# Kernel tuning notes

Measured on AMD Instinct MI355X. Metric: run time of the kernel, lower is better.

The kernel has to match this reference:

```python
import jax, jax.numpy as jnp
import numpy as np

BSZ, SEQ, D, NHEAD, NLAYER, DFF, NQ = 4, 48, 256, 2, 2, 2048, 512
LN_EPS = 1e-5
NEG = jnp.float32(-1e30)


def _layernorm(x, w, b):
    m = jnp.mean(x, axis=-1, keepdims=True)
    v = jnp.mean((x - m) ** 2, axis=-1, keepdims=True)
    return (x - m) / jnp.sqrt(v + LN_EPS) * w + b


def _span_max(x):
    # Cumulative span max: span[b,s,e] = max(x[b,s:e+1]) for e>=s, else 0.
    B, S, H = x.shape
    padded = jnp.concatenate([x, jnp.full((B, S, H), NEG, x.dtype)], axis=1)  # [B,2S,H]

    def step(tmp, i):
        shifted = jax.lax.dynamic_slice(padded, (0, i, 0), (B, S, H))  # x shifted left by i, padded with -inf
        tmp = jnp.maximum(tmp, shifted)  # tmp[b,s] = max(x[b,s:s+i+1])
        return tmp, tmp

    _, ys = jax.lax.scan(step, jnp.full((B, S, H), NEG, x.dtype), jnp.arange(S))
    # ys: [width, B, start, H]; span[b,s,e] = ys[e-s, b, s]
    si = jnp.arange(S)[:, None]
    ei = jnp.arange(S)[None, :]
    w = jnp.clip(ei - si, 0, S - 1)
    span = ys[w, :, jnp.broadcast_to(si, (S, S))]  # [S_start, S_end, B, H]
    span = jnp.where((ei >= si)[:, :, None, None], span, 0.0)
    return span.transpose(2, 0, 1, 3)  # [B,S,S,H]


def _mha(x, wi, bi, wo, bo, kpm):
    # x: [B,T,D]; kpm: [B,T] bool, True = masked key
    B, T, Dm = x.shape
    hd = Dm // NHEAD
    qkv = x @ wi.T + bi
    q, k, v = jnp.split(qkv, 3, axis=-1)
    rs = lambda a: a.reshape(B, T, NHEAD, hd).transpose(0, 2, 1, 3)
    q, k, v = rs(q), rs(k), rs(v)
    scores = jnp.einsum('bhqd,bhkd->bhqk', q, k) * (1.0 / np.sqrt(hd))
    scores = jnp.where(kpm[:, None, None, :], -1e9, scores)
    p = jax.nn.softmax(scores, axis=-1)
    o = jnp.einsum('bhqk,bhkd->bhqd', p, v).transpose(0, 2, 1, 3).reshape(B, T, Dm)
    return o @ wo.T + bo


def _encoder(x, kpm, iw, ib, ow, ob, l1w, l1b, l2w, l2b, f1w, f1b, f2w, f2b, fw, fb):
    # Post-norm torch TransformerEncoder (eval mode, relu, no dropout)
    for l in range(NLAYER):
        a = _mha(x, iw[l], ib[l], ow[l], ob[l], kpm)
        x = _layernorm(x + a, l1w[l], l1b[l])
        f = jax.nn.relu(x @ f1w[l].T + f1b[l]) @ f2w[l].T + f2b[l]
        x = _layernorm(x + f, l2w[l], l2b[l])
    return _layernorm(x, fw, fb)


def _forward(enc, iw, ib, ow, ob, l1w, l1b, l2w, l2b, f1w, f1b, f2w, f2b, fw, fb, s1, e1, qb, s2, e2):
    span = _span_max(enc)  # [B,S,S,D]
    idx = jnp.arange(SEQ)
    kpm2d = idx[None, :] < idx[:, None]  # [start,end]: True where end < start
    kpm = jnp.broadcast_to(kpm2d.reshape(1, SEQ * SEQ), (BSZ, SEQ * SEQ))
    out = _encoder(span.reshape(BSZ, SEQ * SEQ, D), kpm, iw, ib, ow, ob, l1w, l1b, l2w, l2b, f1w, f1b, f2w, f2b, fw, fb)
    out = out.reshape(BSZ, SEQ, SEQ, D)
    res1 = out[qb, s1, e1]
    res2 = out[qb, s2, e2]
    return res1, res2


def setup_inputs() -> dict:
    key = jax.random.key(0)
    ks = jax.random.split(key, 16)
    sc = 0.02
    enc = jax.random.normal(ks[0], (BSZ, SEQ, D), jnp.float32)
    inp = {
        'encoded_input': enc,
        'in_proj_w': jax.random.normal(ks[1], (NLAYER, 3 * D, D), jnp.float32) * sc,
        'in_proj_b': jnp.zeros((NLAYER, 3 * D), jnp.float32),
        'out_proj_w': jax.random.normal(ks[2], (NLAYER, D, D), jnp.float32) * sc,
        'out_proj_b': jnp.zeros((NLAYER, D), jnp.float32),
        'ln1_w': jnp.ones((NLAYER, D), jnp.float32),
        'ln1_b': jnp.zeros((NLAYER, D), jnp.float32),
        'ln2_w': jnp.ones((NLAYER, D), jnp.float32),
        'ln2_b': jnp.zeros((NLAYER, D), jnp.float32),
        'ff1_w': jax.random.normal(ks[3], (NLAYER, DFF, D), jnp.float32) * sc,
        'ff1_b': jnp.zeros((NLAYER, DFF), jnp.float32),
        'ff2_w': jax.random.normal(ks[4], (NLAYER, D, DFF), jnp.float32) * sc,
        'ff2_b': jnp.zeros((NLAYER, D), jnp.float32),
        'fln_w': jnp.ones((D,), jnp.float32),
        'fln_b': jnp.zeros((D,), jnp.float32),
    }
    s1 = jax.random.randint(ks[5], (NQ,), 0, SEQ)
    e1 = jnp.minimum(s1 + jax.random.randint(ks[6], (NQ,), 0, SEQ), SEQ - 1)
    s2 = jax.random.randint(ks[7], (NQ,), 0, SEQ)
    e2 = jnp.minimum(s2 + jax.random.randint(ks[8], (NQ,), 0, SEQ), SEQ - 1)
    inp['start_ids_1'] = s1
    inp['end_ids_1'] = e1
    inp['query_batch_idx'] = jax.random.randint(ks[9], (NQ,), 0, BSZ)
    inp['start_ids_2'] = s2
    inp['end_ids_2'] = e2
    return inp


def reference(encoded_input, in_proj_w, in_proj_b, out_proj_w, out_proj_b, ln1_w, ln1_b, ln2_w, ln2_b, ff1_w, ff1_b, ff2_w, ff2_b, fln_w, fln_b, start_ids_1, end_ids_1, query_batch_idx, start_ids_2, end_ids_2):
    return _forward(encoded_input, in_proj_w, in_proj_b, out_proj_w, out_proj_b, ln1_w, ln1_b, ln2_w, ln2_b, ff1_w, ff1_b, ff2_w, ff2_b, fln_w, fln_b, start_ids_1, end_ids_1, query_batch_idx, start_ids_2, end_ids_2)
```

## Files before the change

kernel.cpp:

```cpp
#include <hip/hip_runtime.h>
#include <hip/hip_bf16.h>

#define BSZ 4
#define SEQ 48
#define DMODEL 256
#define NHEAD 2
#define HD 128
#define NLAYERS 2
#define DFF_C 2048
#define NQ_C 512
#define NV 1176
#define NTOT (BSZ * NV)
#define NVP 1216
#define KSPLIT 5
#define FSPLIT 4
#define OSPLIT 2
#define SCALE 0.088388347648318447f

typedef unsigned short u16;
typedef __attribute__((ext_vector_type(8))) short bf16x8;
typedef __attribute__((ext_vector_type(4))) float f32x4;

__device__ inline u16 f2b(float f) {
    __hip_bfloat16 h = __float2bfloat16(f);
    return *reinterpret_cast<u16*>(&h);
}
__device__ inline void storeval(float* p, float v) { *p = v; }
__device__ inline void storeval(u16* p, float v) { *p = f2b(v); }

__global__ __launch_bounds__(256) void castspan_kernel(
    const float* __restrict__ iw, const float* __restrict__ ow,
    const float* __restrict__ f1w, const float* __restrict__ f2w,
    u16* __restrict__ iwb, u16* __restrict__ owb,
    u16* __restrict__ f1wb, u16* __restrict__ f2wb,
    const float* __restrict__ enc, float* __restrict__ X,
    u16* __restrict__ Xb) {
    int bid = blockIdx.x;
    if (bid < 2560) {
        int i = bid * 256 + threadIdx.x;
        const float* src;
        u16* dst;
        int off;
        if (i < 98304)       { src = iw;  dst = iwb;  off = i; }
        else if (i < 131072) { src = ow;  dst = owb;  off = i - 98304; }
        else if (i < 393216) { src = f1w; dst = f1wb; off = i - 131072; }
        else                 { src = f2w; dst = f2wb; off = i - 393216; }
        float4 v = *(const float4*)(src + (size_t)off * 4);
        *(ushort4*)(dst + (size_t)off * 4) =
            make_ushort4(f2b(v.x), f2b(v.y), f2b(v.z), f2b(v.w));
    } else {
        int sb = bid - 2560;
        int i = sb % SEQ, b = sb / SEQ, h = threadIdx.x;
        int tb = i * SEQ - (i * (i - 1)) / 2 - i;
        float run = -1e30f;
        for (int j = i; j < SEQ; ++j) {
            run = fmaxf(run, enc[((size_t)b * SEQ + j) * DMODEL + h]);
            size_t idx = ((size_t)b * NV + tb + j) * DMODEL + h;
            X[idx] = run;
            Xb[idx] = f2b(run);
        }
    }
}

template <typename OutT, bool RELU>
__global__ __launch_bounds__(256) void mm_kernel(
    const u16* __restrict__ A, const u16* __restrict__ W,
    const float* __restrict__ bias, const float* __restrict__ Res,
    OutT* __restrict__ C, int N, int K, int lda, int ldw, int ldc,
    float alpha, int WV, int KC, int splitRows) {
    __shared__ u16 As[64][72];
    __shared__ u16 Ws[64][72];
    const float4 fz = make_float4(0.f, 0.f, 0.f, 0.f);
    int ks = blockIdx.z;
    int kb = ks * KC, ke = min(K, kb + KC);
    if (splitRows) C += (size_t)ks * splitRows * ldc;
    int p0 = blockIdx.x * 64, n0 = blockIdx.y * 64;
    int tid = threadIdx.x, lane = tid & 63, w = tid >> 6;
    int col_l = lane & 15, quad = lane >> 4;
    f32x4 acc[4] = {};
    for (int k0 = kb; k0 < ke; k0 += 64) {
        int r = tid >> 2, seg = (tid & 3) * 16;
        {
            int gn = n0 + r;
            const u16* ap = A + (size_t)gn * lda + k0 + seg;
            float4 a0 = fz, a1 = fz;
            if (gn < N) { a0 = *(const float4*)ap; a1 = *(const float4*)(ap + 8); }
            *(float4*)&As[r][seg] = a0;
            *(float4*)&As[r][seg + 8] = a1;
        }
        {
            int gp = p0 + r;
            const u16* wp = W + (size_t)gp * ldw + k0 + seg;
            float4 w0 = fz, w1 = fz;
            if (gp < WV) { w0 = *(const float4*)wp; w1 = *(const float4*)(wp + 8); }
            *(float4*)&Ws[r][seg] = w0;
            *(float4*)&Ws[r][seg + 8] = w1;
        }
        __syncthreads();
        bf16x8 a0 = *(const bf16x8*)&As[w * 16 + col_l][quad * 8];
        bf16x8 a1 = *(const bf16x8*)&As[w * 16 + col_l][32 + quad * 8];
#pragma unroll
        for (int c = 0; c < 4; ++c) {
            bf16x8 b0 = *(const bf16x8*)&Ws[c * 16 + col_l][quad * 8];
            bf16x8 b1 = *(const bf16x8*)&Ws[c * 16 + col_l][32 + quad * 8];
            acc[c] = __builtin_amdgcn_mfma_f32_16x16x32_bf16(a0, b0, acc[c], 0, 0, 0);
            acc[c] = __builtin_amdgcn_mfma_f32_16x16x32_bf16(a1, b1, acc[c], 0, 0, 0);
        }
        __syncthreads();
    }
#pragma unroll
    for (int c = 0; c < 4; ++c) {
        int col = p0 + c * 16 + col_l;
        float bv = bias ? bias[col] : 0.f;
#pragma unroll
        for (int reg = 0; reg < 4; ++reg) {
            int row = n0 + w * 16 + quad * 4 + reg;
            if (row < N) {
                float v = acc[c][reg] * alpha + bv;
                if (Res) v += Res[(size_t)row * ldc + col];
                if (RELU) v = fmaxf(v, 0.f);
                storeval(&C[(size_t)row * ldc + col], v);
            }
        }
    }
}

template <typename OutT, bool RELU>
__global__ __launch_bounds__(256) void mmw_kernel(
    const u16* __restrict__ A, const u16* __restrict__ W,
    const float* __restrict__ bias,
    OutT* __restrict__ C, int N, int K, int lda, int ldw, int ldc,
    int WV, int KC, int splitRows) {
    __shared__ u16 As[64][72];
    __shared__ u16 Ws[128][72];
    const float4 fz = make_float4(0.f, 0.f, 0.f, 0.f);
    int ks = blockIdx.z;
    int kb = ks * KC, ke = min(K, kb + KC);
    if (splitRows) C += (size_t)ks * splitRows * ldc;
    int p0 = blockIdx.x * 128, n0 = blockIdx.y * 64;
    int tid = threadIdx.x, lane = tid & 63, w = tid >> 6;
    int col_l = lane & 15, quad = lane >> 4;
    f32x4 acc[8] = {};
    for (int k0 = kb; k0 < ke; k0 += 64) {
        {
            int r = tid >> 2, seg = (tid & 3) * 16;
            int gn = n0 + r;
            const u16* ap = A + (size_t)gn * lda + k0 + seg;
            float4 a0 = fz, a1 = fz;
            if (gn < N) { a0 = *(const float4*)ap; a1 = *(const float4*)(ap + 8); }
            *(float4*)&As[r][seg] = a0;
            *(float4*)&As[r][seg + 8] = a1;
        }
        {
            int r2 = tid >> 1, seg2 = (tid & 1) * 32;
            int gp = p0 + r2;
            const u16* wp = W + (size_t)gp * ldw + k0 + seg2;
#pragma unroll
            for (int j = 0; j < 4; ++j) {
                float4 wv = fz;
                if (gp < WV) wv = *(const float4*)(wp + j * 8);
                *(float4*)&Ws[r2][seg2 + j * 8] = wv;
            }
        }
        __syncthreads();
        bf16x8 a0 = *(const bf16x8*)&As[w * 16 + col_l][quad * 8];
        bf16x8 a1 = *(const bf16x8*)&As[w * 16 + col_l][32 + quad * 8];
#pragma unroll
        for (int c = 0; c < 8; ++c) {
            bf16x8 b0 = *(const bf16x8*)&Ws[c * 16 + col_l][quad * 8];
            bf16x8 b1 = *(const bf16x8*)&Ws[c * 16 + col_l][32 + quad * 8];
            acc[c] = __builtin_amdgcn_mfma_f32_16x16x32_bf16(a0, b0, acc[c], 0, 0, 0);
            acc[c] = __builtin_amdgcn_mfma_f32_16x16x32_bf16(a1, b1, acc[c], 0, 0, 0);
        }
        __syncthreads();
    }
#pragma unroll
    for (int c = 0; c < 8; ++c) {
        int col = p0 + c * 16 + col_l;
        float bv = bias ? bias[col] : 0.f;
#pragma unroll
        for (int reg = 0; reg < 4; ++reg) {
            int row = n0 + w * 16 + quad * 4 + reg;
            if (row < N) {
                float v = acc[c][reg] + bv;
                if (RELU) v = fmaxf(v, 0.f);
                storeval(&C[(size_t)row * ldc + col], v);
            }
        }
    }
}

__global__ __launch_bounds__(256) void vtrans_kernel(const u16* __restrict__ QKVb,
                                                     u16* __restrict__ VT) {
    __shared__ u16 T[64][66];
    const float4 fz = make_float4(0.f, 0.f, 0.f, 0.f);
    int kt = blockIdx.x, dt = blockIdx.y, bh = blockIdx.z;
    int b = bh >> 1, h = bh & 1;
    size_t rb = (size_t)b * NV;
    int tid = threadIdx.x;
    {
        int r = tid >> 2, cs = (tid & 3) * 16;
        int key = kt * 64 + r;
        float4 v0 = fz, v1 = fz;
        if (key < NV) {
            const u16* vp = QKVb + (rb + key) * 768 + 2 * DMODEL + h * HD + dt * 64 + cs;
            v0 = *(const float4*)vp;
            v1 = *(const float4*)(vp + 8);
        }
        *(float4*)&T[r][cs] = v0;
        *(float4*)&T[r][cs + 8] = v1;
    }
    __syncthreads();
    {
        int dl = tid >> 2, ks2 = (tid & 3) * 16;
        u16 tmp[16];
#pragma unroll
        for (int j = 0; j < 16; ++j) tmp[j] = T[ks2 + j][dl];
        u16* dst = VT + ((size_t)bh * HD + dt * 64 + dl) * NVP + kt * 64 + ks2;
        *(float4*)dst = *(float4*)&tmp[0];
        *(float4*)(dst + 8) = *(float4*)&tmp[8];
    }
}

__global__ __launch_bounds__(256) void flash_kernel(const u16* __restrict__ QKVb,
                                                    const u16* __restrict__ VT,
                                                    float* __restrict__ Opart,
                                                    float* __restrict__ ML) {
    __shared__ u16 Ks[64][136];
    __shared__ u16 Vt[128][72];
    __shared__ u16 Ps[4][16][72];
    const float4 fz = make_float4(0.f, 0.f, 0.f, 0.f);
    int tid = threadIdx.x, lane = tid & 63, w = tid >> 6;
    int col_l = lane & 15, quad = lane >> 4;
    int bh = blockIdx.y, b = bh >> 1, h = bh & 1;
    int ks = blockIdx.z;
    int t0 = ks * 4, tcnt = min(4, 19 - t0);
    size_t rb = (size_t)b * NV;
    int q0 = blockIdx.x * 64, wq0 = q0 + w * 16;

    float4 qv[4];
    {
        int qrow = wq0 + col_l;
        if (qrow < NV) {
            const u16* qp = QKVb + (rb + qrow) * 768 + h * HD + quad * 8;
#pragma unroll
            for (int kf = 0; kf < 4; ++kf) qv[kf] = *(const float4*)(qp + kf * 32);
        } else {
#pragma unroll
            for (int kf = 0; kf < 4; ++kf) qv[kf] = fz;
        }
    }

    f32x4 oacc[8] = {};
    float m_run[4], l_run[4];
#pragma unroll
    for (int r = 0; r < 4; ++r) { m_run[r] = -1e30f; l_run[r] = 0.f; }

    for (int it = 0; it < tcnt; ++it) {
        int kt = (t0 + it) * 64;
        {
            int r = tid >> 2, seg = (tid & 3) * 32;
            int key = kt + r;
            const u16* kp = QKVb + (rb + key) * 768 + DMODEL + h * HD + seg;
#pragma unroll
            for (int t4 = 0; t4 < 4; ++t4) {
                float4 v = fz;
                if (key < NV) v = *(const float4*)(kp + t4 * 8);
                *(float4*)&Ks[r][seg + t4 * 8] = v;
            }
        }
        {
            int d = tid >> 1, half = (tid & 1) * 32;
            const u16* vp = VT + ((size_t)bh * HD + d) * NVP + kt + half;
#pragma unroll
            for (int t4 = 0; t4 < 4; ++t4)
                *(float4*)&Vt[d][half + t4 * 8] = *(const float4*)(vp + t4 * 8);
        }
        __syncthreads();

        f32x4 s[4] = {};
#pragma unroll
        for (int c = 0; c < 4; ++c)
#pragma unroll
            for (int kf = 0; kf < 4; ++kf) {
                bf16x8 kfr = *(const bf16x8*)&Ks[c * 16 + col_l][kf * 32 + quad * 8];
                s[c] = __builtin_amdgcn_mfma_f32_16x16x32_bf16(
                    *(const bf16x8*)&qv[kf], kfr, s[c], 0, 0, 0);
            }

        float pv[4][4];
#pragma unroll
        for (int c = 0; c < 4; ++c) {
            bool kvalid = (kt + c * 16 + col_l) < NV;
#pragma unroll
            for (int r = 0; r < 4; ++r)
                pv[c][r] = kvalid ? s[c][r] * SCALE : -1e30f;
        }
        float al[4];
#pragma unroll
        for (int r = 0; r < 4; ++r) {
            float mx = fmaxf(fmaxf(pv[0][r], pv[1][r]), fmaxf(pv[2][r], pv[3][r]));
#pragma unroll
            for (int off = 1; off < 16; off <<= 1)
                mx = fmaxf(mx, __shfl_xor(mx, off));
            float mn = fmaxf(m_run[r], mx);
            al[r] = __expf(m_run[r] - mn);
            m_run[r] = mn;
            float sum = 0.f;
#pragma unroll
            for (int c = 0; c < 4; ++c) {
                float p = __expf(pv[c][r] - mn);
                pv[c][r] = p;
                sum += p;
            }
#pragma unroll
            for (int off = 1; off < 16; off <<= 1) sum += __shfl_xor(sum, off);
            l_run[r] = l_run[r] * al[r] + sum;
        }
#pragma unroll
        for (int ct = 0; ct < 8; ++ct)
#pragma unroll
            for (int r = 0; r < 4; ++r) oacc[ct][r] *= al[r];

#pragma unroll
        for (int c = 0; c < 4; ++c)
#pragma unroll
            for (int r = 0; r < 4; ++r)
                Ps[w][quad * 4 + r][c * 16 + col_l] = f2b(pv[c][r]);
        bf16x8 pf0 = *(const bf16x8*)&Ps[w][col_l][quad * 8];
        bf16x8 pf1 = *(const bf16x8*)&Ps[w][col_l][32 + quad * 8];
#pragma unroll
        for (int ct = 0; ct < 8; ++ct) {
            bf16x8 v0 = *(const bf16x8*)&Vt[ct * 16 + col_l][quad * 8];
            bf16x8 v1 = *(const bf16x8*)&Vt[ct * 16 + col_l][32 + quad * 8];
            oacc[ct] = __builtin_amdgcn_mfma_f32_16x16x32_bf16(pf0, v0, oacc[ct], 0, 0, 0);
            oacc[ct] = __builtin_amdgcn_mfma_f32_16x16x32_bf16(pf1, v1, oacc[ct], 0, 0, 0);
        }
        __syncthreads();
    }

    size_t slab = (size_t)(ks * 8 + bh) * NVP;
#pragma unroll
    for (int ct = 0; ct < 8; ++ct)
#pragma unroll
        for (int r = 0; r < 4; ++r) {
            int row = wq0 + quad * 4 + r;
            Opart[(slab + row) * HD + ct * 16 + col_l] = oacc[ct][r];
        }
    if (col_l == 0) {
#pragma unroll
        for (int r = 0; r < 4; ++r) {
            int row = wq0 + quad * 4 + r;
            ML[(slab + row) * 2 + 0] = m_run[r];
            ML[(slab + row) * 2 + 1] = l_run[r];
        }
    }
}

__global__ __launch_bounds__(256) void comb_kernel(const float* __restrict__ Opart,
                                                   const float* __restrict__ ML,
                                                   u16* __restrict__ Obuf) {
    int bh = blockIdx.y, b = bh >> 1, h = bh & 1;
    int tid = threadIdx.x;
    int row = blockIdx.x * 2 + (tid >> 7);
    int d = tid & 127;
    if (row >= NV) return;
    float m[KSPLIT], l[KSPLIT];
#pragma unroll
    for (int i = 0; i < KSPLIT; ++i) {
        size_t mb = ((size_t)(i * 8 + bh) * NVP + row) * 2;
        m[i] = ML[mb];
        l[i] = ML[mb + 1];
    }
    float M = m[0];
#pragma unroll
    for (int i = 1; i < KSPLIT; ++i) M = fmaxf(M, m[i]);
    float wsum = 0.f, o = 0.f;
#pragma unroll
    for (int i = 0; i < KSPLIT; ++i) {
        float wi = __expf(m[i] - M);
        wsum += l[i] * wi;
        o += Opart[((size_t)(i * 8 + bh) * NVP + row) * HD + d] * wi;
    }
    Obuf[((size_t)b * NV + row) * DMODEL + h * HD + d] = f2b(o / wsum);
}

template <int NSLAB>
__global__ __launch_bounds__(256) void redln_kernel(const float* __restrict__ Xres,
                                                    const float* __restrict__ P,
                                                    const float* __restrict__ cbias,
                                                    const float* __restrict__ w,
                                                    const float* __restrict__ bb,
                                                    float* __restrict__ Y,
                                                    u16* __restrict__ Yb) {
    int wv = threadIdx.x >> 6, lane = threadIdx.x & 63;
    int r = blockIdx.x * 4 + wv;
    size_t base = (size_t)r * DMODEL + lane * 4;
    float4 v = *(const float4*)(Xres + base);
    float4 c4 = *(const float4*)(cbias + lane * 4);
    v.x += c4.x; v.y += c4.y; v.z += c4.z; v.w += c4.w;
#pragma unroll
    for (int z = 0; z < NSLAB; ++z) {
        float4 p4 = *(const float4*)(P + (size_t)z * NTOT * DMODEL + base);
        v.x += p4.x; v.y += p4.y; v.z += p4.z; v.w += p4.w;
    }
    float s1 = v.x + v.y + v.z + v.w;
    float s2 = v.x * v.x + v.y * v.y + v.z * v.z + v.w * v.w;
#pragma unroll
    for (int off = 32; off > 0; off >>= 1) {
        s1 += __shfl_xor(s1, off);
        s2 += __shfl_xor(s2, off);
    }
    float mean = s1 * (1.f / DMODEL);
    float var = s2 * (1.f / DMODEL) - mean * mean;
    float rstd = rsqrtf(var + 1e-5f);
    float4 w4 = *(const float4*)(w + lane * 4);
    float4 b4 = *(const float4*)(bb + lane * 4);
    float o0 = (v.x - mean) * rstd * w4.x + b4.x;
    float o1 = (v.y - mean) * rstd * w4.y + b4.y;
    float o2 = (v.z - mean) * rstd * w4.z + b4.z;
    float o3 = (v.w - mean) * rstd * w4.w + b4.w;
    *(float4*)(Y + base) = make_float4(o0, o1, o2, o3);
    *(ushort4*)(Yb + base) = make_ushort4(f2b(o0), f2b(o1), f2b(o2), f2b(o3));
}

__global__ __launch_bounds__(64) void gatherln_kernel(const float* __restrict__ X,
                                                      const float* __restrict__ fw,
                                                      const float* __restrict__ fb,
                                                      const int* __restrict__ s1,
                                                      const int* __restrict__ e1,
                                                      const int* __restrict__ qb,
                                                      const int* __restrict__ s2,
                                                      const int* __restrict__ e2,
                                                      float* __restrict__ out) {
    int q = blockIdx.x, which = blockIdx.y, lane = threadIdx.x;
    int s = which ? s2[q] : s1[q];
    int e = which ? e2[q] : e1[q];
    int b = qb[q];
    int t = s * SEQ - (s * (s - 1)) / 2 + (e - s);
    if (t < 0) t = 0;
    if (t >= NV) t = NV - 1;
    size_t base = ((size_t)b * NV + t) * DMODEL + lane * 4;
    float4 v = *(const float4*)(X + base);
    float s1v = v.x + v.y + v.z + v.w;
    float s2v = v.x * v.x + v.y * v.y + v.z * v.z + v.w * v.w;
#pragma unroll
    for (int off = 32; off > 0; off >>= 1) {
        s1v += __shfl_xor(s1v, off);
        s2v += __shfl_xor(s2v, off);
    }
    float mean = s1v * (1.f / DMODEL);
    float var = s2v * (1.f / DMODEL) - mean * mean;
    float rstd = rsqrtf(var + 1e-5f);
    float4 w4 = *(const float4*)(fw + lane * 4);
    float4 b4 = *(const float4*)(fb + lane * 4);
    float o0 = (v.x - mean) * rstd * w4.x + b4.x;
    float o1 = (v.y - mean) * rstd * w4.y + b4.y;
    float o2 = (v.z - mean) * rstd * w4.z + b4.z;
    float o3 = (v.w - mean) * rstd * w4.w + b4.w;
    *(float4*)(out + ((size_t)which * NQ_C + q) * DMODEL + lane * 4) =
        make_float4(o0, o1, o2, o3);
}

extern "C" void kernel_launch(void* const* d_in, const int* in_sizes, int n_in,
                              void* d_out, int out_size, void* d_ws, size_t ws_size,
                              hipStream_t stream) {
    const float* enc = (const float*)d_in[0];
    const float* iw  = (const float*)d_in[1];
    const float* ib  = (const float*)d_in[2];
    const float* ow  = (const float*)d_in[3];
    const float* ob  = (const float*)d_in[4];
    const float* l1w = (const float*)d_in[5];
    const float* l1b = (const float*)d_in[6];
    const float* l2w = (const float*)d_in[7];
    const float* l2b = (const float*)d_in[8];
    const float* f1w = (const float*)d_in[9];
    const float* f1b = (const float*)d_in[10];
    const float* f2w = (const float*)d_in[11];
    const float* f2b_ = (const float*)d_in[12];
    const float* flw = (const float*)d_in[13];
    const float* flb = (const float*)d_in[14];
    const int* s1 = (const int*)d_in[15];
    const int* e1 = (const int*)d_in[16];
    const int* qb = (const int*)d_in[17];
    const int* s2 = (const int*)d_in[18];
    const int* e2 = (const int*)d_in[19];
    float* out = (float*)d_out;

    char* p = (char*)d_ws;
    float* X     = (float*)p;  p += (size_t)NTOT * DMODEL * 4;
    u16* Xb      = (u16*)p;    p += (size_t)NTOT * DMODEL * 2;
    u16* Obuf    = (u16*)p;    p += (size_t)NTOT * DMODEL * 2;
    u16* QKVb    = (u16*)p;    p += (size_t)NTOT * 3 * DMODEL * 2;
    u16* VT      = (u16*)p;    p += (size_t)8 * HD * NVP * 2;
    float* ML    = (float*)p;  p += (size_t)KSPLIT * 8 * NVP * 2 * 4;
    float* Opart = (float*)p;  p += (size_t)KSPLIT * 8 * NVP * HD * 4;
    float* Pbuf  = (float*)p;  p += (size_t)FSPLIT * NTOT * DMODEL * 4;
    u16* wb      = (u16*)p;
    u16* F1b     = (u16*)Opart;

    u16* iwb  = wb;
    u16* owb  = iwb + 2 * 3 * DMODEL * DMODEL;
    u16* f1wb = owb + 2 * DMODEL * DMODEL;
    u16* f2wb = f1wb + 2 * DFF_C * DMODEL;

    castspan_kernel<<<dim3(2752), 256, 0, stream>>>(iw, ow, f1w, f2w,
                                                    iwb, owb, f1wb, f2wb,
                                                    enc, X, Xb);

    for (int l = 0; l < NLAYERS; ++l) {
        mm_kernel<u16, false><<<dim3(12, 74, 1), 256, 0, stream>>>(
            Xb, iwb + (size_t)l * 3 * DMODEL * DMODEL, ib + (size_t)l * 3 * DMODEL,
            nullptr, QKVb, NTOT, DMODEL, DMODEL, DMODEL, 3 * DMODEL, 1.f,
            3 * DMODEL, DMODEL, 0);
        vtrans_kernel<<<dim3(19, 2, 8), 256, 0, stream>>>(QKVb, VT);
        flash_kernel<<<dim3(19, 8, KSPLIT), 256, 0, stream>>>(QKVb, VT, Opart, ML);
        comb_kernel<<<dim3(588, 8), 256, 0, stream>>>(Opart, ML, Obuf);
        mm_kernel<float, false><<<dim3(4, 74, OSPLIT), 256, 0, stream>>>(
            Obuf, owb + (size_t)l * DMODEL * DMODEL, nullptr, nullptr, Pbuf,
            NTOT, DMODEL, DMODEL, DMODEL, DMODEL, 1.f, DMODEL,
            DMODEL / OSPLIT, NTOT);
        redln_kernel<OSPLIT><<<dim3(NTOT / 4), 256, 0, stream>>>(
            X, Pbuf, ob + (size_t)l * DMODEL,
            l1w + (size_t)l * DMODEL, l1b + (size_t)l * DMODEL, X, Xb);
        mmw_kernel<u16, true><<<dim3(16, 74, 1), 256, 0, stream>>>(
            Xb, f1wb + (size_t)l * DFF_C * DMODEL, f1b + (size_t)l * DFF_C,
            F1b, NTOT, DMODEL, DMODEL, DMODEL, DFF_C, DFF_C, DMODEL, 0);
        mmw_kernel<float, false><<<dim3(2, 74, FSPLIT), 256, 0, stream>>>(
            F1b, f2wb + (size_t)l * DMODEL * DFF_C, nullptr, Pbuf,
            NTOT, DFF_C, DFF_C, DFF_C, DMODEL, DMODEL, DFF_C / FSPLIT, NTOT);
        redln_kernel<FSPLIT><<<dim3(NTOT / 4), 256, 0, stream>>>(
            X, Pbuf, f2b_ + (size_t)l * DMODEL,
            l2w + (size_t)l * DMODEL, l2b + (size_t)l * DMODEL, X, Xb);
    }
    gatherln_kernel<<<dim3(NQ_C, 2), 64, 0, stream>>>(X, flw, flb,
                                                      s1, e1, qb, s2, e2, out);
}
```

Baseline: 316.7 us.

## Fuse V transpose into QKV GEMM, lazy softmax rescale, fuse final LN into gather

```diff
diff --git a/kernel.cpp b/kernel.cpp
--- a/kernel.cpp
+++ b/kernel.cpp
@@ -34,7 +34,7 @@
     u16* __restrict__ iwb, u16* __restrict__ owb,
     u16* __restrict__ f1wb, u16* __restrict__ f2wb,
     const float* __restrict__ enc, float* __restrict__ X,
-    u16* __restrict__ Xb) {
+    u16* __restrict__ Xb, u16* __restrict__ VT) {
     int bid = blockIdx.x;
     if (bid < 2560) {
         int i = bid * 256 + threadIdx.x;
@@ -48,7 +48,7 @@
         float4 v = *(const float4*)(src + (size_t)off * 4);
         *(ushort4*)(dst + (size_t)off * 4) =
             make_ushort4(f2b(v.x), f2b(v.y), f2b(v.z), f2b(v.w));
-    } else {
+    } else if (bid < 2752) {
         int sb = bid - 2560;
         int i = sb % SEQ, b = sb / SEQ, h = threadIdx.x;
         int tb = i * SEQ - (i * (i - 1)) / 2 - i;
@@ -59,14 +59,19 @@
             X[idx] = run;
             Xb[idx] = f2b(run);
         }
-    }
-}
-
-template <typename OutT, bool RELU>
+    } else {
+        int i = (bid - 2752) * 256 + threadIdx.x;
+        int row = i / 20, off = i % 20;
+        ((unsigned int*)VT)[(size_t)row * (NVP / 2) + (NV / 2) + off] = 0u;
+    }
+}
+
+template <typename OutT, bool RELU, bool VOUT>
 __global__ __launch_bounds__(256) void mm_kernel(
     const u16* __restrict__ A, const u16* __restrict__ W,
     const float* __restrict__ bias, const float* __restrict__ Res,
-    OutT* __restrict__ C, int N, int K, int lda, int ldw, int ldc,
+    OutT* __restrict__ C, u16* __restrict__ VTout,
+    int N, int K, int lda, int ldw, int ldc,
     float alpha, int WV, int KC, int splitRows) {
     __shared__ u16 As[64][72];
     __shared__ u16 Ws[64][72];
@@ -108,19 +113,32 @@
         }
         __syncthreads();
     }
+    int row0 = n0 + w * 16 + quad * 4;
 #pragma unroll
     for (int c = 0; c < 4; ++c) {
         int col = p0 + c * 16 + col_l;
         float bv = bias ? bias[col] : 0.f;
+        float vv[4];
 #pragma unroll
         for (int reg = 0; reg < 4; ++reg) {
-            int row = n0 + w * 16 + quad * 4 + reg;
-            if (row < N) {
-                float v = acc[c][reg] * alpha + bv;
-                if (Res) v += Res[(size_t)row * ldc + col];
-                if (RELU) v = fmaxf(v, 0.f);
-                storeval(&C[(size_t)row * ldc + col], v);
-            }
+            int row = row0 + reg;
+            float v = acc[c][reg] * alpha + bv;
+            if (Res && row < N) v += Res[(size_t)row * ldc + col];
+            if (RELU) v = fmaxf(v, 0.f);
+            vv[reg] = v;
+        }
+        if (VOUT && col >= 2 * DMODEL) {
+            if (row0 < N) {
+                int b = row0 / NV, t = row0 - b * NV;
+                int d = col - 2 * DMODEL;
+                *(ushort4*)(VTout + ((size_t)(b * 2 + (d >> 7)) * HD + (d & 127)) * NVP + t) =
+                    make_ushort4(f2b(vv[0]), f2b(vv[1]), f2b(vv[2]), f2b(vv[3]));
+            }
+        } else {
+#pragma unroll
+            for (int reg = 0; reg < 4; ++reg)
+                if (row0 + reg < N)
+                    storeval(&C[(size_t)(row0 + reg) * ldc + col], vv[reg]);
         }
     }
 }
@@ -190,38 +208,6 @@
     }
 }
 
-__global__ __launch_bounds__(256) void vtrans_kernel(const u16* __restrict__ QKVb,
-                                                     u16* __restrict__ VT) {
-    __shared__ u16 T[64][66];
-    const float4 fz = make_float4(0.f, 0.f, 0.f, 0.f);
-    int kt = blockIdx.x, dt = blockIdx.y, bh = blockIdx.z;
-    int b = bh >> 1, h = bh & 1;
-    size_t rb = (size_t)b * NV;
-    int tid = threadIdx.x;
-    {
-        int r = tid >> 2, cs = (tid & 3) * 16;
-        int key = kt * 64 + r;
-        float4 v0 = fz, v1 = fz;
-        if (key < NV) {
-            const u16* vp = QKVb + (rb + key) * 768 + 2 * DMODEL + h * HD + dt * 64 + cs;
-            v0 = *(const float4*)vp;
-            v1 = *(const float4*)(vp + 8);
-        }
-        *(float4*)&T[r][cs] = v0;
-        *(float4*)&T[r][cs + 8] = v1;
-    }
-    __syncthreads();
-    {
-        int dl = tid >> 2, ks2 = (tid & 3) * 16;
-        u16 tmp[16];
-#pragma unroll
-        for (int j = 0; j < 16; ++j) tmp[j] = T[ks2 + j][dl];
-        u16* dst = VT + ((size_t)bh * HD + dt * 64 + dl) * NVP + kt * 64 + ks2;
-        *(float4*)dst = *(float4*)&tmp[0];
-        *(float4*)(dst + 8) = *(float4*)&tmp[8];
-    }
-}
-
 __global__ __launch_bounds__(256) void flash_kernel(const u16* __restrict__ QKVb,
                                                     const u16* __restrict__ VT,
                                                     float* __restrict__ Opart,
@@ -296,31 +282,41 @@
             for (int r = 0; r < 4; ++r)
                 pv[c][r] = kvalid ? s[c][r] * SCALE : -1e30f;
         }
-        float al[4];
+        float mxv[4];
+        int need = 0;
 #pragma unroll
         for (int r = 0; r < 4; ++r) {
             float mx = fmaxf(fmaxf(pv[0][r], pv[1][r]), fmaxf(pv[2][r], pv[3][r]));
 #pragma unroll
             for (int off = 1; off < 16; off <<= 1)
                 mx = fmaxf(mx, __shfl_xor(mx, off));
-            float mn = fmaxf(m_run[r], mx);
-            al[r] = __expf(m_run[r] - mn);
-            m_run[r] = mn;
+            mxv[r] = mx;
+            need |= (mx > m_run[r] + 8.f) ? 1 : 0;
+        }
+        if (__any(need)) {
+#pragma unroll
+            for (int r = 0; r < 4; ++r) {
+                float mn = fmaxf(m_run[r], mxv[r]);
+                float al = __expf(m_run[r] - mn);
+                m_run[r] = mn;
+                l_run[r] *= al;
+#pragma unroll
+                for (int ct = 0; ct < 8; ++ct) oacc[ct][r] *= al;
+            }
+        }
+#pragma unroll
+        for (int r = 0; r < 4; ++r) {
             float sum = 0.f;
 #pragma unroll
             for (int c = 0; c < 4; ++c) {
-                float p = __expf(pv[c][r] - mn);
-                pv[c][r] = p;
-                sum += p;
+                float pp = __expf(pv[c][r] - m_run[r]);
+                pv[c][r] = pp;
+                sum += pp;
             }
 #pragma unroll
             for (int off = 1; off < 16; off <<= 1) sum += __shfl_xor(sum, off);
-            l_run[r] = l_run[r] * al[r] + sum;
-        }
-#pragma unroll
-        for (int ct = 0; ct < 8; ++ct)
-#pragma unroll
-            for (int r = 0; r < 4; ++r) oacc[ct][r] *= al[r];
+            l_run[r] += sum;
+        }
 
 #pragma unroll
         for (int c = 0; c < 4; ++c)
@@ -424,15 +420,19 @@
     *(ushort4*)(Yb + base) = make_ushort4(f2b(o0), f2b(o1), f2b(o2), f2b(o3));
 }
 
-__global__ __launch_bounds__(64) void gatherln_kernel(const float* __restrict__ X,
-                                                      const float* __restrict__ fw,
-                                                      const float* __restrict__ fb,
-                                                      const int* __restrict__ s1,
-                                                      const int* __restrict__ e1,
-                                                      const int* __restrict__ qb,
-                                                      const int* __restrict__ s2,
-                                                      const int* __restrict__ e2,
-                                                      float* __restrict__ out) {
+__global__ __launch_bounds__(64) void gatherln2_kernel(const float* __restrict__ Xres,
+                                                       const float* __restrict__ P,
+                                                       const float* __restrict__ cbias,
+                                                       const float* __restrict__ w2,
+                                                       const float* __restrict__ b2,
+                                                       const float* __restrict__ fw,
+                                                       const float* __restrict__ fb,
+                                                       const int* __restrict__ s1,
+                                                       const int* __restrict__ e1,
+                                                       const int* __restrict__ qb,
+                                                       const int* __restrict__ s2,
+                                                       const int* __restrict__ e2,
+                                                       float* __restrict__ out) {
     int q = blockIdx.x, which = blockIdx.y, lane = threadIdx.x;
     int s = which ? s2[q] : s1[q];
     int e = which ? e2[q] : e1[q];
@@ -441,7 +441,14 @@
     if (t < 0) t = 0;
     if (t >= NV) t = NV - 1;
     size_t base = ((size_t)b * NV + t) * DMODEL + lane * 4;
-    float4 v = *(const float4*)(X + base);
+    float4 v = *(const float4*)(Xres + base);
+    float4 c4 = *(const float4*)(cbias + lane * 4);
+    v.x += c4.x; v.y += c4.y; v.z += c4.z; v.w += c4.w;
+#pragma unroll
+    for (int z = 0; z < FSPLIT; ++z) {
+        float4 p4 = *(const float4*)(P + (size_t)z * NTOT * DMODEL + base);
+        v.x += p4.x; v.y += p4.y; v.z += p4.z; v.w += p4.w;
+    }
     float s1v = v.x + v.y + v.z + v.w;
     float s2v = v.x * v.x + v.y * v.y + v.z * v.z + v.w * v.w;
 #pragma unroll
@@ -452,14 +459,30 @@
     float mean = s1v * (1.f / DMODEL);
     float var = s2v * (1.f / DMODEL) - mean * mean;
     float rstd = rsqrtf(var + 1e-5f);
-    float4 w4 = *(const float4*)(fw + lane * 4);
-    float4 b4 = *(const float4*)(fb + lane * 4);
+    float4 w4 = *(const float4*)(w2 + lane * 4);
+    float4 b4 = *(const float4*)(b2 + lane * 4);
     float o0 = (v.x - mean) * rstd * w4.x + b4.x;
     float o1 = (v.y - mean) * rstd * w4.y + b4.y;
     float o2 = (v.z - mean) * rstd * w4.z + b4.z;
     float o3 = (v.w - mean) * rstd * w4.w + b4.w;
+    float t1 = o0 + o1 + o2 + o3;
+    float t2 = o0 * o0 + o1 * o1 + o2 * o2 + o3 * o3;
+#pragma unroll
+    for (int off = 32; off > 0; off >>= 1) {
+        t1 += __shfl_xor(t1, off);
+        t2 += __shfl_xor(t2, off);
+    }
+    float mean2 = t1 * (1.f / DMODEL);
+    float var2 = t2 * (1.f / DMODEL) - mean2 * mean2;
+    float rstd2 = rsqrtf(var2 + 1e-5f);
+    float4 fw4 = *(const float4*)(fw + lane * 4);
+    float4 fb4 = *(const float4*)(fb + lane * 4);
+    float r0 = (o0 - mean2) * rstd2 * fw4.x + fb4.x;
+    float r1 = (o1 - mean2) * rstd2 * fw4.y + fb4.y;
+    float r2 = (o2 - mean2) * rstd2 * fw4.z + fb4.z;
+    float r3 = (o3 - mean2) * rstd2 * fw4.w + fb4.w;
     *(float4*)(out + ((size_t)which * NQ_C + q) * DMODEL + lane * 4) =
-        make_float4(o0, o1, o2, o3);
+        make_float4(r0, r1, r2, r3);
 }
 
 extern "C" void kernel_launch(void* const* d_in, const int* in_sizes, int n_in,
@@ -504,21 +527,20 @@
     u16* f1wb = owb + 2 * DMODEL * DMODEL;
     u16* f2wb = f1wb + 2 * DFF_C * DMODEL;
 
-    castspan_kernel<<<dim3(2752), 256, 0, stream>>>(iw, ow, f1w, f2w,
+    castspan_kernel<<<dim3(2832), 256, 0, stream>>>(iw, ow, f1w, f2w,
                                                     iwb, owb, f1wb, f2wb,
-                                                    enc, X, Xb);
+                                                    enc, X, Xb, VT);
 
     for (int l = 0; l < NLAYERS; ++l) {
-        mm_kernel<u16, false><<<dim3(12, 74, 1), 256, 0, stream>>>(
+        mm_kernel<u16, false, true><<<dim3(12, 74, 1), 256, 0, stream>>>(
             Xb, iwb + (size_t)l * 3 * DMODEL * DMODEL, ib + (size_t)l * 3 * DMODEL,
-            nullptr, QKVb, NTOT, DMODEL, DMODEL, DMODEL, 3 * DMODEL, 1.f,
+            nullptr, QKVb, VT, NTOT, DMODEL, DMODEL, DMODEL, 3 * DMODEL, 1.f,
             3 * DMODEL, DMODEL, 0);
-        vtrans_kernel<<<dim3(19, 2, 8), 256, 0, stream>>>(QKVb, VT);
         flash_kernel<<<dim3(19, 8, KSPLIT), 256, 0, stream>>>(QKVb, VT, Opart, ML);
         comb_kernel<<<dim3(588, 8), 256, 0, stream>>>(Opart, ML, Obuf);
-        mm_kernel<float, false><<<dim3(4, 74, OSPLIT), 256, 0, stream>>>(
+        mm_kernel<float, false, false><<<dim3(4, 74, OSPLIT), 256, 0, stream>>>(
             Obuf, owb + (size_t)l * DMODEL * DMODEL, nullptr, nullptr, Pbuf,
-            NTOT, DMODEL, DMODEL, DMODEL, DMODEL, 1.f, DMODEL,
+            nullptr, NTOT, DMODEL, DMODEL, DMODEL, DMODEL, 1.f, DMODEL,
             DMODEL / OSPLIT, NTOT);
         redln_kernel<OSPLIT><<<dim3(NTOT / 4), 256, 0, stream>>>(
             X, Pbuf, ob + (size_t)l * DMODEL,
@@ -529,10 +551,15 @@
         mmw_kernel<float, false><<<dim3(2, 74, FSPLIT), 256, 0, stream>>>(
             F1b, f2wb + (size_t)l * DMODEL * DFF_C, nullptr, Pbuf,
             NTOT, DFF_C, DFF_C, DFF_C, DMODEL, DMODEL, DFF_C / FSPLIT, NTOT);
-        redln_kernel<FSPLIT><<<dim3(NTOT / 4), 256, 0, stream>>>(
-            X, Pbuf, f2b_ + (size_t)l * DMODEL,
-            l2w + (size_t)l * DMODEL, l2b + (size_t)l * DMODEL, X, Xb);
-    }
-    gatherln_kernel<<<dim3(NQ_C, 2), 64, 0, stream>>>(X, flw, flb,
-                                                      s1, e1, qb, s2, e2, out);
-}
+        if (l < NLAYERS - 1) {
+            redln_kernel<FSPLIT><<<dim3(NTOT / 4), 256, 0, stream>>>(
+                X, Pbuf, f2b_ + (size_t)l * DMODEL,
+                l2w + (size_t)l * DMODEL, l2b + (size_t)l * DMODEL, X, Xb);
+        } else {
+            gatherln2_kernel<<<dim3(NQ_C, 2), 64, 0, stream>>>(
+                X, Pbuf, f2b_ + (size_t)l * DMODEL,
+                l2w + (size_t)l * DMODEL, l2b + (size_t)l * DMODEL,
+                flw, flb, s1, e1, qb, s2, e2, out);
+        }
+    }
+}
```

Measured after the change: 299.1 us. 1.06x faster.
